# Kernel optimization log

Hardware: AMD Instinct MI355X
Metric: run time of the kernel (lower is better)

## Reference

```python
import jax, jax.numpy as jnp
import numpy as np

B, T, IN_DIM = 32, 1024, 32
E, H, P = 256, 4, 32  # embed_dim, heads, max_patches
HD = E // H


def _lin(x, w, b):
    # torch nn.Linear: y = x @ W.T + b, W: [out, in]
    return jnp.einsum('...i,oi->...o', x, w) + b


def setup_inputs() -> dict:
    key = jax.random.key(0)
    ks = jax.random.split(key, 13)
    s = 0.02
    return {
        'x': jax.random.normal(ks[0], (B, T, IN_DIM), jnp.float32),
        'ip_w': jax.random.normal(ks[1], (E, IN_DIM), jnp.float32) * s,
        'ip_b': jnp.zeros((E,), jnp.float32),
        'in_proj_w': jax.random.normal(ks[2], (3 * E, E), jnp.float32) * s,
        'in_proj_b': jnp.zeros((3 * E,), jnp.float32),
        'out_w': jax.random.normal(ks[3], (E, E), jnp.float32) * s,
        'out_b': jnp.zeros((E,), jnp.float32),
        'bp_w1': jax.random.normal(ks[4], (32, E), jnp.float32) * s,
        'bp_b1': jnp.zeros((32,), jnp.float32),
        'bp_w2': jax.random.normal(ks[5], (1, 32), jnp.float32) * s,
        'bp_b2': jnp.zeros((1,), jnp.float32),
        'pr_w': jax.random.normal(ks[6], (E, E), jnp.float32) * s,
        'pr_b': jnp.zeros((E,), jnp.float32),
    }


def reference(x, ip_w, ip_b, in_proj_w, in_proj_b, out_w, out_b,
              bp_w1, bp_b1, bp_w2, bp_b2, pr_w, pr_b):
    # input projection
    h = _lin(x, ip_w, ip_b)  # [B,T,E]
    # MultiheadAttention (self-attn, batch_first, eval/no-dropout)
    qkv = _lin(h, in_proj_w, in_proj_b)  # [B,T,3E]
    q, k, v = jnp.split(qkv, 3, axis=-1)
    q = q.reshape(B, T, H, HD)
    k = k.reshape(B, T, H, HD)
    v = v.reshape(B, T, H, HD)
    scores = jnp.einsum('bqhd,bkhd->bhqk', q, k) / jnp.sqrt(jnp.float32(HD))
    attn = jax.nn.softmax(scores, axis=-1)
    ctx = jnp.einsum('bhqk,bkhd->bqhd', attn, v).reshape(B, T, E)
    attn_out = _lin(ctx, out_w, out_b)  # [B,T,E]
    # boundary scores
    bscore = jax.nn.sigmoid(_lin(jax.nn.relu(_lin(attn_out, bp_w1, bp_b1)), bp_w2, bp_b2))[..., 0]  # [B,T]
    cbp = jnp.cumsum(bscore, axis=1)
    cbp = cbp / (cbp[:, -1:] + 1e-6)
    pid = jnp.minimum(jnp.floor(cbp * P).astype(jnp.int32), P - 1)  # [B,T]
    # segment-mean pooling via scatter-add
    b_idx = jnp.broadcast_to(jnp.arange(B)[:, None], (B, T))
    pe = jnp.zeros((B, P, E), attn_out.dtype).at[b_idx, pid].add(attn_out)
    cnt = jnp.zeros((B, P), attn_out.dtype).at[b_idx, pid].add(1.0)
    pe = pe / jnp.clip(cnt, 1.0)[..., None]
    return _lin(pe, pr_w, pr_b)  # [B,P,E]
```

## Files before the change

kernel.cpp:

```cpp
#include <hip/hip_runtime.h>
#include <math.h>

constexpr int Bn  = 32;
constexpr int Tn  = 1024;
constexpr int INn = 32;
constexpr int En  = 256;
constexpr int Pn  = 32;

typedef short bf16x8 __attribute__((ext_vector_type(8)));
typedef float f32x4  __attribute__((ext_vector_type(4)));

__device__ __forceinline__ unsigned short f2bf(float f) {
    unsigned int b = __float_as_uint(f);
    b += 0x7FFF + ((b >> 16) & 1);
    return (unsigned short)(b >> 16);
}
__device__ __forceinline__ float bf2f(unsigned short h) {
    return __uint_as_float(((unsigned int)h) << 16);
}
__device__ __forceinline__ unsigned int permpack(float lo, float hi) {
    return __builtin_amdgcn_perm(__float_as_uint(hi), __float_as_uint(lo),
                                 0x07060302u);
}

__global__ __launch_bounds__(256) void k_prep(const float* __restrict__ ipw,
                                              const float* __restrict__ ipb,
                                              const float* __restrict__ inw,
                                              const float* __restrict__ inb,
                                              const float* __restrict__ outw,
                                              const float* __restrict__ w1,
                                              const float* __restrict__ prw,
                                              unsigned short* __restrict__ Wcb,
                                              float* __restrict__ bc,
                                              unsigned short* __restrict__ Wb,
                                              unsigned short* __restrict__ w1h,
                                              unsigned short* __restrict__ w1l,
                                              unsigned short* __restrict__ pwh,
                                              unsigned short* __restrict__ pwl) {
    int blk = blockIdx.x, tid = threadIdx.x;
    if (blk < 96) {
        int idx = blk * 256 + tid;
        int o = idx >> 5, i = idx & 31;
        const float* wr = inw + (size_t)o * En;
        float a0 = 0.f, a1 = 0.f;
        for (int e = 0; e < En; e += 2) {
            a0 += wr[e]     * ipw[(size_t)e * INn + i];
            a1 += wr[e + 1] * ipw[(size_t)(e + 1) * INn + i];
        }
        Wcb[(size_t)o * INn + i] = f2bf(a0 + a1);
    } else if (blk < 99) {
        int o = (blk - 96) * 256 + tid;
        const float* wr = inw + (size_t)o * En;
        float a = inb[o];
        for (int e = 0; e < En; ++e) a += wr[e] * ipb[e];
        bc[o] = a;
    } else if (blk < 163) {
        int idx = (blk - 99) * 256 + tid;
        float4 a = *(const float4*)(outw + (size_t)idx * 4);
        unsigned int u0 = f2bf(a.x) | ((unsigned int)f2bf(a.y) << 16);
        unsigned int u1 = f2bf(a.z) | ((unsigned int)f2bf(a.w) << 16);
        *(uint2*)(Wb + (size_t)idx * 4) = make_uint2(u0, u1);
    } else if (blk < 195) {
        int idx = (blk - 163) * 256 + tid;
        float a = w1[idx];
        unsigned short h = f2bf(a);
        w1h[idx] = h;
        w1l[idx] = f2bf(a - bf2f(h));
    } else {
        int idx = (blk - 195) * 256 + tid;
        float a = prw[idx];
        unsigned short h = f2bf(a);
        pwh[idx] = h;
        pwl[idx] = f2bf(a - bf2f(h));
    }
}

__global__ __launch_bounds__(256, 2) void k_qkv(const float* __restrict__ x,
                                                const unsigned short* __restrict__ Wcb,
                                                const float* __restrict__ bc,
                                                unsigned short* __restrict__ Qb,
                                                unsigned short* __restrict__ Kb,
                                                unsigned short* __restrict__ Vt) {
    int tid = threadIdx.x;
    int wv = tid >> 6, lane = tid & 63;
    int cl = lane & 15, quad = lane >> 4;
    int m0 = blockIdx.x * 64;
    int b = m0 >> 10, tl0 = m0 & 1023;
    int n0w = wv * 192;
    f32x4 zero4 = {0.f, 0.f, 0.f, 0.f};

    bf16x8 wfrag[12]; float bv[12];
#pragma unroll
    for (int nt = 0; nt < 12; ++nt) {
        int col = n0w + nt * 16 + cl;
        wfrag[nt] = *(const bf16x8*)(Wcb + (size_t)col * 32 + quad * 8);
        bv[nt] = bc[col];
    }
#pragma unroll
    for (int mt = 0; mt < 4; ++mt) {
        const float* xr = x + (size_t)(m0 + mt * 16 + cl) * 32 + quad * 8;
        float4 xa = *(const float4*)xr, xc = *(const float4*)(xr + 4);
        bf16x8 af;
        af[0] = (short)f2bf(xa.x); af[1] = (short)f2bf(xa.y);
        af[2] = (short)f2bf(xa.z); af[3] = (short)f2bf(xa.w);
        af[4] = (short)f2bf(xc.x); af[5] = (short)f2bf(xc.y);
        af[6] = (short)f2bf(xc.z); af[7] = (short)f2bf(xc.w);
        f32x4 acc[12];
#pragma unroll
        for (int nt = 0; nt < 12; ++nt)
            acc[nt] = __builtin_amdgcn_mfma_f32_16x16x32_bf16(af, wfrag[nt], zero4, 0, 0, 0);
        int tloc = tl0 + mt * 16 + quad * 4;
#pragma unroll
        for (int nt = 0; nt < 12; ++nt) {
            int col = n0w + nt * 16 + cl;
            int slot = col >> 8, c = col & 255;
            int h = c >> 6, d = c & 63;
            int bh = b * 4 + h;
            if (slot == 2) {
                unsigned int u0 = f2bf(acc[nt][0] + bv[nt]) |
                                  ((unsigned int)f2bf(acc[nt][1] + bv[nt]) << 16);
                unsigned int u1 = f2bf(acc[nt][2] + bv[nt]) |
                                  ((unsigned int)f2bf(acc[nt][3] + bv[nt]) << 16);
                *(uint2*)(Vt + ((size_t)bh * 64 + d) * 1024 + tloc) = make_uint2(u0, u1);
            } else {
                unsigned short* dst = (slot ? Kb : Qb) +
                                      ((size_t)bh * 1024 + tloc) * 64 + d;
#pragma unroll
                for (int r = 0; r < 4; ++r)
                    dst[(size_t)r * 64] = f2bf(acc[nt][r] + bv[nt]);
            }
        }
    }
}

__global__ __launch_bounds__(256, 4) void k_attn(const unsigned short* __restrict__ Qb,
                                                 const unsigned short* __restrict__ Kb,
                                                 const unsigned short* __restrict__ Vt,
                                                 unsigned short* __restrict__ Po0,
                                                 unsigned short* __restrict__ Po1,
                                                 float* __restrict__ L0,
                                                 float* __restrict__ L1) {
    __shared__ unsigned short Ks[64][72];
    __shared__ unsigned short Vs[64][72];
    __shared__ __align__(16) unsigned short Pl[4][2][16][40];
    int blk = blockIdx.x;
    int bh = blk & 127;
    int r_ = blk >> 7;
    int qb = r_ & 7, half = r_ >> 3;
    int b = bh >> 2, h = bh & 3;
    int tid = threadIdx.x;
    int wv = tid >> 6, lane = tid & 63;
    int cl = lane & 15, quad = lane >> 4;
    int qbase = qb * 128 + wv * 32;

    f32x4 zero4 = {0.f, 0.f, 0.f, 0.f};
    bf16x8 qfrag[2][2];
#pragma unroll
    for (int tt = 0; tt < 2; ++tt)
#pragma unroll
        for (int ch = 0; ch < 2; ++ch)
            qfrag[tt][ch] = *(const bf16x8*)(Qb +
                ((size_t)bh * 1024 + qbase + tt * 16 + cl) * 64 + ch * 32 + quad * 8);
    f32x4 acc[2][4];
#pragma unroll
    for (int tt = 0; tt < 2; ++tt)
#pragma unroll
        for (int dt = 0; dt < 4; ++dt) acc[tt][dt] = zero4;
    float l[2] = {0.f, 0.f};

    const unsigned short* Kbase = Kb + (size_t)bh * 65536;
    const unsigned short* Vbase = Vt + (size_t)bh * 65536;

    for (int kt = 0; kt < 8; ++kt) {
        int ktt = half * 8 + kt;
#pragma unroll
        for (int r = 0; r < 2; ++r) {
            int idx = r * 256 + tid; int row = idx >> 3, c16 = idx & 7;
            *(uint4*)&Ks[row][c16 * 8] =
                *(const uint4*)(Kbase + (size_t)(ktt * 64 + row) * 64 + c16 * 8);
            *(uint4*)&Vs[row][c16 * 8] =
                *(const uint4*)(Vbase + (size_t)row * 1024 + ktt * 64 + c16 * 8);
        }
        __syncthreads();
#pragma unroll
        for (int c = 0; c < 2; ++c) {
            bf16x8 ka0 = *(const bf16x8*)&Ks[c * 32 + cl][quad * 8];
            bf16x8 ka1 = *(const bf16x8*)&Ks[c * 32 + cl][32 + quad * 8];
            bf16x8 kb0 = *(const bf16x8*)&Ks[c * 32 + 16 + cl][quad * 8];
            bf16x8 kb1 = *(const bf16x8*)&Ks[c * 32 + 16 + cl][32 + quad * 8];
            bf16x8 va[4];
#pragma unroll
            for (int dt = 0; dt < 4; ++dt)
                va[dt] = *(const bf16x8*)&Vs[dt * 16 + cl][c * 32 + quad * 8];
#pragma unroll
            for (int tt = 0; tt < 2; ++tt) {
                f32x4 s0 = __builtin_amdgcn_mfma_f32_16x16x32_bf16(ka0, qfrag[tt][0], zero4, 0, 0, 0);
                s0 = __builtin_amdgcn_mfma_f32_16x16x32_bf16(ka1, qfrag[tt][1], s0, 0, 0, 0);
                f32x4 s1 = __builtin_amdgcn_mfma_f32_16x16x32_bf16(kb0, qfrag[tt][0], zero4, 0, 0, 0);
                s1 = __builtin_amdgcn_mfma_f32_16x16x32_bf16(kb1, qfrag[tt][1], s1, 0, 0, 0);
                float p0 = __expf(0.125f * s0[0]), p1 = __expf(0.125f * s0[1]);
                float p2 = __expf(0.125f * s0[2]), p3 = __expf(0.125f * s0[3]);
                float p4 = __expf(0.125f * s1[0]), p5 = __expf(0.125f * s1[1]);
                float p6 = __expf(0.125f * s1[2]), p7 = __expf(0.125f * s1[3]);
                unsigned int w0 = permpack(p0, p1);
                unsigned int w1 = permpack(p2, p3);
                unsigned int w2 = permpack(p4, p5);
                unsigned int w3 = permpack(p6, p7);
                l[tt] += ((__uint_as_float(w0 << 16) + __uint_as_float(w0 & 0xffff0000u)) +
                          (__uint_as_float(w1 << 16) + __uint_as_float(w1 & 0xffff0000u))) +
                         ((__uint_as_float(w2 << 16) + __uint_as_float(w2 & 0xffff0000u)) +
                          (__uint_as_float(w3 << 16) + __uint_as_float(w3 & 0xffff0000u)));
                *(uint2*)&Pl[wv][tt][cl][quad * 4]      = make_uint2(w0, w1);
                *(uint2*)&Pl[wv][tt][cl][16 + quad * 4] = make_uint2(w2, w3);
            }
            asm volatile("s_waitcnt lgkmcnt(0)" ::: "memory");
#pragma unroll
            for (int tt = 0; tt < 2; ++tt) {
                bf16x8 pf = *(const bf16x8*)&Pl[wv][tt][cl][quad * 8];
#pragma unroll
                for (int dt = 0; dt < 4; ++dt)
                    acc[tt][dt] = __builtin_amdgcn_mfma_f32_16x16x32_bf16(pf, va[dt], acc[tt][dt], 0, 0, 0);
            }
        }
        __syncthreads();
    }
#pragma unroll
    for (int tt = 0; tt < 2; ++tt) {
        l[tt] += __shfl_xor(l[tt], 16);
        l[tt] += __shfl_xor(l[tt], 32);
    }
    unsigned short* Po = half ? Po1 : Po0;
    float* Lp = half ? L1 : L0;
#pragma unroll
    for (int tt = 0; tt < 2; ++tt) {
#pragma unroll
        for (int r = 0; r < 4; ++r) {
            size_t row = (size_t)(b * 1024 + qbase + tt * 16 + quad * 4 + r) * En;
#pragma unroll
            for (int dt = 0; dt < 4; ++dt)
                Po[row + h * 64 + dt * 16 + cl] = f2bf(acc[tt][dt][r]);
        }
    }
    if (quad == 0) {
#pragma unroll
        for (int tt = 0; tt < 2; ++tt)
            Lp[bh * 1024 + qbase + tt * 16 + cl] = l[tt];
    }
}

__global__ __launch_bounds__(256) void k_out(const unsigned short* __restrict__ Po0,
                                             const unsigned short* __restrict__ Po1,
                                             const float* __restrict__ L0,
                                             const float* __restrict__ L1,
                                             const unsigned short* __restrict__ Wb,
                                             const float* __restrict__ bias,
                                             float* __restrict__ AO) {
    __shared__ unsigned short As[64][32];
    __shared__ unsigned short Bs[256][32];
    int tid = threadIdx.x;
    int wv = tid >> 6, lane = tid & 63;
    int cl = lane & 15, quad = lane >> 4;
    size_t m0 = (size_t)blockIdx.x * 64;

    f32x4 acc[4][4];
#pragma unroll
    for (int mt = 0; mt < 4; ++mt)
#pragma unroll
        for (int nt = 0; nt < 4; ++nt) acc[mt][nt] = {0.f, 0.f, 0.f, 0.f};

    for (int kt = 0; kt < 8; ++kt) {
        if (kt) __syncthreads();
        {
            int row = tid >> 2, c4 = tid & 3;
            size_t g = (m0 + row) * En + kt * 32 + c4 * 8;
            uint4 u0 = *(const uint4*)(Po0 + g);
            uint4 u1 = *(const uint4*)(Po1 + g);
            int gt = (int)(m0 + row);
            int li = ((gt >> 10) * 4 + (kt >> 1)) * 1024 + (gt & 1023);
            float linv = 1.f / (L0[li] + L1[li]);
            unsigned int a0[4] = {u0.x, u0.y, u0.z, u0.w};
            unsigned int a1[4] = {u1.x, u1.y, u1.z, u1.w};
            unsigned int w[4];
#pragma unroll
            for (int j = 0; j < 4; ++j) {
                float lo = (bf2f((unsigned short)(a0[j] & 0xffff)) +
                            bf2f((unsigned short)(a1[j] & 0xffff))) * linv;
                float hi = (bf2f((unsigned short)(a0[j] >> 16)) +
                            bf2f((unsigned short)(a1[j] >> 16))) * linv;
                w[j] = f2bf(lo) | ((unsigned int)f2bf(hi) << 16);
            }
            *(uint4*)&As[row][c4 * 8] = make_uint4(w[0], w[1], w[2], w[3]);
        }
#pragma unroll
        for (int j = 0; j < 4; ++j) {
            int lin = j * 256 + tid; int n = lin >> 2, c = lin & 3;
            *(uint4*)&Bs[n][c * 8] =
                *(const uint4*)(Wb + (size_t)n * En + kt * 32 + c * 8);
        }
        __syncthreads();
        bf16x8 af[4], bfr[4];
#pragma unroll
        for (int mt = 0; mt < 4; ++mt)
            af[mt] = *(const bf16x8*)&As[mt * 16 + cl][quad * 8];
#pragma unroll
        for (int nt = 0; nt < 4; ++nt)
            bfr[nt] = *(const bf16x8*)&Bs[wv * 64 + nt * 16 + cl][quad * 8];
#pragma unroll
        for (int mt = 0; mt < 4; ++mt)
#pragma unroll
            for (int nt = 0; nt < 4; ++nt)
                acc[mt][nt] = __builtin_amdgcn_mfma_f32_16x16x32_bf16(af[mt], bfr[nt], acc[mt][nt], 0, 0, 0);
    }
    float bv[4];
#pragma unroll
    for (int nt = 0; nt < 4; ++nt) bv[nt] = bias[wv * 64 + nt * 16 + cl];
#pragma unroll
    for (int mt = 0; mt < 4; ++mt)
#pragma unroll
        for (int nt = 0; nt < 4; ++nt)
#pragma unroll
            for (int r = 0; r < 4; ++r)
                AO[(m0 + mt * 16 + quad * 4 + r) * En + wv * 64 + nt * 16 + cl] =
                    acc[mt][nt][r] + bv[nt];
}

__global__ __launch_bounds__(256) void k_bscore(const float* __restrict__ AO,
                                                const unsigned short* __restrict__ w1h,
                                                const unsigned short* __restrict__ w1l,
                                                const float* __restrict__ b1,
                                                const float* __restrict__ w2,
                                                const float* __restrict__ b2,
                                                float* __restrict__ bsc) {
    __shared__ unsigned short Ah[128][72];
    __shared__ unsigned short Al[128][72];
    int tid = threadIdx.x;
    int wv = tid >> 6, lane = tid & 63;
    int cl = lane & 15, quad = lane >> 4;
    int m0 = blockIdx.x * 128;

    f32x4 acc[2][2];
#pragma unroll
    for (int mt = 0; mt < 2; ++mt)
#pragma unroll
        for (int nt = 0; nt < 2; ++nt) acc[mt][nt] = {0.f, 0.f, 0.f, 0.f};

    for (int kt = 0; kt < 4; ++kt) {
        if (kt) __syncthreads();
#pragma unroll
        for (int j = 0; j < 8; ++j) {
            int lin = j * 256 + tid; int row = lin >> 4, c4 = lin & 15;
            float4 a = *(const float4*)(AO + (size_t)(m0 + row) * En + kt * 64 + c4 * 4);
            unsigned short h0 = f2bf(a.x), h1v = f2bf(a.y), h2 = f2bf(a.z), h3 = f2bf(a.w);
            unsigned short l0 = f2bf(a.x - bf2f(h0)), l1v = f2bf(a.y - bf2f(h1v));
            unsigned short l2 = f2bf(a.z - bf2f(h2)), l3 = f2bf(a.w - bf2f(h3));
            *(uint2*)&Ah[row][c4 * 4] =
                make_uint2(h0 | ((unsigned int)h1v << 16), h2 | ((unsigned int)h3 << 16));
            *(uint2*)&Al[row][c4 * 4] =
                make_uint2(l0 | ((unsigned int)l1v << 16), l2 | ((unsigned int)l3 << 16));
        }
        __syncthreads();
#pragma unroll
        for (int ks = 0; ks < 2; ++ks) {
            bf16x8 bh_[2], bl_[2];
#pragma unroll
            for (int nt = 0; nt < 2; ++nt) {
                size_t off = (size_t)(nt * 16 + cl) * En + kt * 64 + ks * 32 + quad * 8;
                bh_[nt] = *(const bf16x8*)(w1h + off);
                bl_[nt] = *(const bf16x8*)(w1l + off);
            }
#pragma unroll
            for (int mt = 0; mt < 2; ++mt) {
                int row = wv * 32 + mt * 16 + cl;
                bf16x8 ah = *(const bf16x8*)&Ah[row][ks * 32 + quad * 8];
                bf16x8 al = *(const bf16x8*)&Al[row][ks * 32 + quad * 8];
#pragma unroll
                for (int nt = 0; nt < 2; ++nt) {
                    acc[mt][nt] = __builtin_amdgcn_mfma_f32_16x16x32_bf16(ah, bh_[nt], acc[mt][nt], 0, 0, 0);
                    acc[mt][nt] = __builtin_amdgcn_mfma_f32_16x16x32_bf16(ah, bl_[nt], acc[mt][nt], 0, 0, 0);
                    acc[mt][nt] = __builtin_amdgcn_mfma_f32_16x16x32_bf16(al, bh_[nt], acc[mt][nt], 0, 0, 0);
                }
            }
        }
    }
    float b1v[2], w2v[2];
#pragma unroll
    for (int nt = 0; nt < 2; ++nt) {
        b1v[nt] = b1[nt * 16 + cl];
        w2v[nt] = w2[nt * 16 + cl];
    }
    float b2v = b2[0];
#pragma unroll
    for (int mt = 0; mt < 2; ++mt) {
        f32x4 z;
#pragma unroll
        for (int r = 0; r < 4; ++r)
            z[r] = fmaxf(acc[mt][0][r] + b1v[0], 0.f) * w2v[0] +
                   fmaxf(acc[mt][1][r] + b1v[1], 0.f) * w2v[1];
#pragma unroll
        for (int d = 1; d < 16; d <<= 1)
#pragma unroll
            for (int r = 0; r < 4; ++r) z[r] += __shfl_xor(z[r], d);
        if (cl == 0) {
#pragma unroll
            for (int r = 0; r < 4; ++r)
                bsc[m0 + wv * 32 + mt * 16 + quad * 4 + r] =
                    1.f / (1.f + __expf(-(z[r] + b2v)));
        }
    }
}

__global__ __launch_bounds__(1024) void k_scan(const float* __restrict__ bsc,
                                               int* __restrict__ segs) {
    __shared__ float wsum[16];
    __shared__ float s_pre[1024];
    __shared__ float s_tot;
    int b = blockIdx.x, t = threadIdx.x;
    float x = bsc[b * Tn + t];
#pragma unroll
    for (int d = 1; d < 64; d <<= 1) {
        float y = __shfl_up(x, d);
        if ((t & 63) >= d) x += y;
    }
    int w = t >> 6;
    if ((t & 63) == 63) wsum[w] = x;
    __syncthreads();
    if (t == 0) {
        float s = 0.f;
        for (int i = 0; i < 16; ++i) { float tmp = wsum[i]; wsum[i] = s; s += tmp; }
        s_tot = s;
    }
    __syncthreads();
    float pre = x + wsum[w];
    s_pre[t] = pre;
    __syncthreads();
    float denom = s_tot + 1e-6f;
    float qv = pre / denom * 32.0f;
    int pid = min((int)floorf(qv), 31);
    int pidprev = -1;
    if (t > 0) {
        float qp = s_pre[t - 1] / denom * 32.0f;
        pidprev = min((int)floorf(qp), 31);
    }
    for (int p = pidprev + 1; p <= pid; ++p) segs[b * 33 + p] = t;
    if (t == 1023)
        for (int p = pid + 1; p <= 32; ++p) segs[b * 33 + p] = Tn;
}

__global__ __launch_bounds__(256) void k_pool(const float* __restrict__ ao,
                                              const int* __restrict__ segs,
                                              float* __restrict__ PE) {
    int b = blockIdx.y, p = blockIdx.x;
    int s = segs[b * 33 + p];
    int e = segs[b * 33 + p + 1];
    int tid = threadIdx.x;
    float sum = 0.f;
    for (int t = s; t < e; ++t)
        sum += ao[((size_t)b * Tn + t) * En + tid];
    PE[(size_t)(b * Pn + p) * En + tid] = sum / fmaxf((float)(e - s), 1.f);
}

__global__ __launch_bounds__(256) void k_final(const float* __restrict__ PE,
                                               const unsigned short* __restrict__ pwh,
                                               const unsigned short* __restrict__ pwl,
                                               const float* __restrict__ prb,
                                               float* __restrict__ out) {
    __shared__ unsigned short Ah[64][40];
    __shared__ unsigned short Al[64][40];
    int tid = threadIdx.x;
    int wv = tid >> 6, lane = tid & 63;
    int cl = lane & 15, quad = lane >> 4;
    int m0 = blockIdx.x * 64;

    f32x4 acc[4][4];
#pragma unroll
    for (int mt = 0; mt < 4; ++mt)
#pragma unroll
        for (int nt = 0; nt < 4; ++nt) acc[mt][nt] = {0.f, 0.f, 0.f, 0.f};

    for (int kt = 0; kt < 8; ++kt) {
        if (kt) __syncthreads();
        {
            int row = tid >> 2, c8 = (tid & 3) * 8;
            const float* src = PE + (size_t)(m0 + row) * En + kt * 32 + c8;
            float4 a = *(const float4*)src, b4 = *(const float4*)(src + 4);
            float v[8] = {a.x, a.y, a.z, a.w, b4.x, b4.y, b4.z, b4.w};
            unsigned int hw[4], lw[4];
#pragma unroll
            for (int j = 0; j < 4; ++j) {
                unsigned short h0 = f2bf(v[2 * j]), h1 = f2bf(v[2 * j + 1]);
                unsigned short q0 = f2bf(v[2 * j] - bf2f(h0));
                unsigned short q1 = f2bf(v[2 * j + 1] - bf2f(h1));
                hw[j] = h0 | ((unsigned int)h1 << 16);
                lw[j] = q0 | ((unsigned int)q1 << 16);
            }
            *(uint4*)&Ah[row][c8] = make_uint4(hw[0], hw[1], hw[2], hw[3]);
            *(uint4*)&Al[row][c8] = make_uint4(lw[0], lw[1], lw[2], lw[3]);
        }
        __syncthreads();
        bf16x8 ah[4], al[4], bh_[4], bl_[4];
#pragma unroll
        for (int mt = 0; mt < 4; ++mt) {
            ah[mt] = *(const bf16x8*)&Ah[mt * 16 + cl][quad * 8];
            al[mt] = *(const bf16x8*)&Al[mt * 16 + cl][quad * 8];
        }
#pragma unroll
        for (int nt = 0; nt < 4; ++nt) {
            size_t off = (size_t)(wv * 64 + nt * 16 + cl) * En + kt * 32 + quad * 8;
            bh_[nt] = *(const bf16x8*)(pwh + off);
            bl_[nt] = *(const bf16x8*)(pwl + off);
        }
#pragma unroll
        for (int mt = 0; mt < 4; ++mt)
#pragma unroll
            for (int nt = 0; nt < 4; ++nt) {
                acc[mt][nt] = __builtin_amdgcn_mfma_f32_16x16x32_bf16(ah[mt], bh_[nt], acc[mt][nt], 0, 0, 0);
                acc[mt][nt] = __builtin_amdgcn_mfma_f32_16x16x32_bf16(ah[mt], bl_[nt], acc[mt][nt], 0, 0, 0);
                acc[mt][nt] = __builtin_amdgcn_mfma_f32_16x16x32_bf16(al[mt], bh_[nt], acc[mt][nt], 0, 0, 0);
            }
    }
    float bv[4];
#pragma unroll
    for (int nt = 0; nt < 4; ++nt) bv[nt] = prb[wv * 64 + nt * 16 + cl];
#pragma unroll
    for (int mt = 0; mt < 4; ++mt)
#pragma unroll
        for (int nt = 0; nt < 4; ++nt)
#pragma unroll
            for (int r = 0; r < 4; ++r)
                out[(size_t)(m0 + mt * 16 + quad * 4 + r) * En + wv * 64 + nt * 16 + cl] =
                    acc[mt][nt][r] + bv[nt];
}

extern "C" void kernel_launch(void* const* d_in, const int* in_sizes, int n_in,
                              void* d_out, int out_size, void* d_ws, size_t ws_size,
                              hipStream_t stream) {
    const float* x    = (const float*)d_in[0];
    const float* ipw  = (const float*)d_in[1];
    const float* ipb  = (const float*)d_in[2];
    const float* inw  = (const float*)d_in[3];
    const float* inb  = (const float*)d_in[4];
    const float* outw = (const float*)d_in[5];
    const float* outb = (const float*)d_in[6];
    const float* bw1  = (const float*)d_in[7];
    const float* bb1  = (const float*)d_in[8];
    const float* bw2  = (const float*)d_in[9];
    const float* bb2  = (const float*)d_in[10];
    const float* prw  = (const float*)d_in[11];
    const float* prb  = (const float*)d_in[12];

    char* base = (char*)d_ws;
    unsigned short* Qb  = (unsigned short*)base;
    unsigned short* Kb  = Qb + (size_t)8388608;
    float*          AO  = (float*)base;
    unsigned short* Vt  = (unsigned short*)(base + (size_t)33554432);
    float*          PE  = (float*)(base + (size_t)33554432);
    unsigned short* Po0 = (unsigned short*)(base + (size_t)50331648);
    unsigned short* Po1 = (unsigned short*)(base + (size_t)67108864);
    unsigned short* Wcb = (unsigned short*)(base + (size_t)83886080);
    float*          bc  = (float*)(base + (size_t)83935232);
    unsigned short* Wb  = (unsigned short*)(base + (size_t)83938304);
    unsigned short* w1h = (unsigned short*)(base + (size_t)84069376);
    unsigned short* w1l = (unsigned short*)(base + (size_t)84085760);
    float*          L0  = (float*)(base + (size_t)84102144);
    float*          L1  = (float*)(base + (size_t)84626432);
    float*          bsc = (float*)(base + (size_t)85150720);
    int*           segs = (int*)(base + (size_t)85281792);
    unsigned short* pwh = (unsigned short*)(base + (size_t)85286912);
    unsigned short* pwl = (unsigned short*)(base + (size_t)85417984);

    k_prep<<<451, 256, 0, stream>>>(ipw, ipb, inw, inb, outw, bw1, prw,
                                    Wcb, bc, Wb, w1h, w1l, pwh, pwl);
    k_qkv<<<512, 256, 0, stream>>>(x, Wcb, bc, Qb, Kb, Vt);
    k_attn<<<2048, 256, 0, stream>>>(Qb, Kb, Vt, Po0, Po1, L0, L1);
    k_out<<<512, 256, 0, stream>>>(Po0, Po1, L0, L1, Wb, outb, AO);
    k_bscore<<<256, 256, 0, stream>>>(AO, w1h, w1l, bb1, bw2, bb2, bsc);
    k_scan<<<32, 1024, 0, stream>>>(bsc, segs);
    k_pool<<<dim3(32, 32), 256, 0, stream>>>(AO, segs, PE);
    k_final<<<16, 256, 0, stream>>>(PE, pwh, pwl, prb, (float*)d_out);
}
```

Before: 218.0 us.

## Fuse boundary MLP into out-proj, scan into pool, weight casts into qkv

```diff
diff --git a/kernel.cpp b/kernel.cpp
--- a/kernel.cpp
+++ b/kernel.cpp
@@ -27,16 +27,8 @@
                                               const float* __restrict__ ipb,
                                               const float* __restrict__ inw,
                                               const float* __restrict__ inb,
-                                              const float* __restrict__ outw,
-                                              const float* __restrict__ w1,
-                                              const float* __restrict__ prw,
                                               unsigned short* __restrict__ Wcb,
-                                              float* __restrict__ bc,
-                                              unsigned short* __restrict__ Wb,
-                                              unsigned short* __restrict__ w1h,
-                                              unsigned short* __restrict__ w1l,
-                                              unsigned short* __restrict__ pwh,
-                                              unsigned short* __restrict__ pwl) {
+                                              float* __restrict__ bc) {
     int blk = blockIdx.x, tid = threadIdx.x;
     if (blk < 96) {
         int idx = blk * 256 + tid;
@@ -48,40 +40,53 @@
             a1 += wr[e + 1] * ipw[(size_t)(e + 1) * INn + i];
         }
         Wcb[(size_t)o * INn + i] = f2bf(a0 + a1);
-    } else if (blk < 99) {
+    } else {
         int o = (blk - 96) * 256 + tid;
         const float* wr = inw + (size_t)o * En;
         float a = inb[o];
         for (int e = 0; e < En; ++e) a += wr[e] * ipb[e];
         bc[o] = a;
-    } else if (blk < 163) {
-        int idx = (blk - 99) * 256 + tid;
-        float4 a = *(const float4*)(outw + (size_t)idx * 4);
-        unsigned int u0 = f2bf(a.x) | ((unsigned int)f2bf(a.y) << 16);
-        unsigned int u1 = f2bf(a.z) | ((unsigned int)f2bf(a.w) << 16);
-        *(uint2*)(Wb + (size_t)idx * 4) = make_uint2(u0, u1);
-    } else if (blk < 195) {
-        int idx = (blk - 163) * 256 + tid;
-        float a = w1[idx];
-        unsigned short h = f2bf(a);
-        w1h[idx] = h;
-        w1l[idx] = f2bf(a - bf2f(h));
-    } else {
-        int idx = (blk - 195) * 256 + tid;
-        float a = prw[idx];
-        unsigned short h = f2bf(a);
-        pwh[idx] = h;
-        pwl[idx] = f2bf(a - bf2f(h));
     }
 }
 
 __global__ __launch_bounds__(256, 2) void k_qkv(const float* __restrict__ x,
                                                 const unsigned short* __restrict__ Wcb,
                                                 const float* __restrict__ bc,
+                                                const float* __restrict__ outw,
+                                                const float* __restrict__ w1,
+                                                const float* __restrict__ prw,
                                                 unsigned short* __restrict__ Qb,
                                                 unsigned short* __restrict__ Kb,
-                                                unsigned short* __restrict__ Vt) {
+                                                unsigned short* __restrict__ Vt,
+                                                unsigned short* __restrict__ Wb,
+                                                unsigned short* __restrict__ w1h,
+                                                unsigned short* __restrict__ w1l,
+                                                unsigned short* __restrict__ pwh,
+                                                unsigned short* __restrict__ pwl) {
     int tid = threadIdx.x;
+    if (blockIdx.x >= 512) {
+        int cb = blockIdx.x - 512;
+        if (cb < 64) {
+            int idx = cb * 256 + tid;
+            float4 a = *(const float4*)(outw + (size_t)idx * 4);
+            unsigned int u0 = f2bf(a.x) | ((unsigned int)f2bf(a.y) << 16);
+            unsigned int u1 = f2bf(a.z) | ((unsigned int)f2bf(a.w) << 16);
+            *(uint2*)(Wb + (size_t)idx * 4) = make_uint2(u0, u1);
+        } else if (cb < 96) {
+            int idx = (cb - 64) * 256 + tid;
+            float a = w1[idx];
+            unsigned short h = f2bf(a);
+            w1h[idx] = h;
+            w1l[idx] = f2bf(a - bf2f(h));
+        } else {
+            int idx = (cb - 96) * 256 + tid;
+            float a = prw[idx];
+            unsigned short h = f2bf(a);
+            pwh[idx] = h;
+            pwl[idx] = f2bf(a - bf2f(h));
+        }
+        return;
+    }
     int wv = tid >> 6, lane = tid & 63;
     int cl = lane & 15, quad = lane >> 4;
     int m0 = blockIdx.x * 64;
@@ -152,6 +157,7 @@
     int wv = tid >> 6, lane = tid & 63;
     int cl = lane & 15, quad = lane >> 4;
     int qbase = qb * 128 + wv * 32;
+    const float SCL = 0.18033688f;
 
     f32x4 zero4 = {0.f, 0.f, 0.f, 0.f};
     bf16x8 qfrag[2][2];
@@ -198,10 +204,10 @@
                 s0 = __builtin_amdgcn_mfma_f32_16x16x32_bf16(ka1, qfrag[tt][1], s0, 0, 0, 0);
                 f32x4 s1 = __builtin_amdgcn_mfma_f32_16x16x32_bf16(kb0, qfrag[tt][0], zero4, 0, 0, 0);
                 s1 = __builtin_amdgcn_mfma_f32_16x16x32_bf16(kb1, qfrag[tt][1], s1, 0, 0, 0);
-                float p0 = __expf(0.125f * s0[0]), p1 = __expf(0.125f * s0[1]);
-                float p2 = __expf(0.125f * s0[2]), p3 = __expf(0.125f * s0[3]);
-                float p4 = __expf(0.125f * s1[0]), p5 = __expf(0.125f * s1[1]);
-                float p6 = __expf(0.125f * s1[2]), p7 = __expf(0.125f * s1[3]);
+                float p0 = exp2f(SCL * s0[0]), p1 = exp2f(SCL * s0[1]);
+                float p2 = exp2f(SCL * s0[2]), p3 = exp2f(SCL * s0[3]);
+                float p4 = exp2f(SCL * s1[0]), p5 = exp2f(SCL * s1[1]);
+                float p6 = exp2f(SCL * s1[2]), p7 = exp2f(SCL * s1[3]);
                 unsigned int w0 = permpack(p0, p1);
                 unsigned int w1 = permpack(p2, p3);
                 unsigned int w2 = permpack(p4, p5);
@@ -254,9 +260,16 @@
                                              const float* __restrict__ L1,
                                              const unsigned short* __restrict__ Wb,
                                              const float* __restrict__ bias,
-                                             float* __restrict__ AO) {
+                                             const unsigned short* __restrict__ w1h,
+                                             const unsigned short* __restrict__ w1l,
+                                             const float* __restrict__ b1,
+                                             const float* __restrict__ w2,
+                                             const float* __restrict__ b2,
+                                             float* __restrict__ AO,
+                                             float* __restrict__ bsc) {
     __shared__ unsigned short As[64][32];
     __shared__ unsigned short Bs[256][32];
+    __shared__ unsigned short Ah[64][258];
     int tid = threadIdx.x;
     int wv = tid >> 6, lane = tid & 63;
     int cl = lane & 15, quad = lane >> 4;
@@ -314,88 +327,39 @@
     float bv[4];
 #pragma unroll
     for (int nt = 0; nt < 4; ++nt) bv[nt] = bias[wv * 64 + nt * 16 + cl];
+    __syncthreads();
 #pragma unroll
     for (int mt = 0; mt < 4; ++mt)
 #pragma unroll
         for (int nt = 0; nt < 4; ++nt)
 #pragma unroll
-            for (int r = 0; r < 4; ++r)
-                AO[(m0 + mt * 16 + quad * 4 + r) * En + wv * 64 + nt * 16 + cl] =
-                    acc[mt][nt][r] + bv[nt];
-}
-
-__global__ __launch_bounds__(256) void k_bscore(const float* __restrict__ AO,
-                                                const unsigned short* __restrict__ w1h,
-                                                const unsigned short* __restrict__ w1l,
-                                                const float* __restrict__ b1,
-                                                const float* __restrict__ w2,
-                                                const float* __restrict__ b2,
-                                                float* __restrict__ bsc) {
-    __shared__ unsigned short Ah[128][72];
-    __shared__ unsigned short Al[128][72];
-    int tid = threadIdx.x;
-    int wv = tid >> 6, lane = tid & 63;
-    int cl = lane & 15, quad = lane >> 4;
-    int m0 = blockIdx.x * 128;
-
-    f32x4 acc[2][2];
-#pragma unroll
-    for (int mt = 0; mt < 2; ++mt)
-#pragma unroll
-        for (int nt = 0; nt < 2; ++nt) acc[mt][nt] = {0.f, 0.f, 0.f, 0.f};
-
-    for (int kt = 0; kt < 4; ++kt) {
-        if (kt) __syncthreads();
-#pragma unroll
-        for (int j = 0; j < 8; ++j) {
-            int lin = j * 256 + tid; int row = lin >> 4, c4 = lin & 15;
-            float4 a = *(const float4*)(AO + (size_t)(m0 + row) * En + kt * 64 + c4 * 4);
-            unsigned short h0 = f2bf(a.x), h1v = f2bf(a.y), h2 = f2bf(a.z), h3 = f2bf(a.w);
-            unsigned short l0 = f2bf(a.x - bf2f(h0)), l1v = f2bf(a.y - bf2f(h1v));
-            unsigned short l2 = f2bf(a.z - bf2f(h2)), l3 = f2bf(a.w - bf2f(h3));
-            *(uint2*)&Ah[row][c4 * 4] =
-                make_uint2(h0 | ((unsigned int)h1v << 16), h2 | ((unsigned int)h3 << 16));
-            *(uint2*)&Al[row][c4 * 4] =
-                make_uint2(l0 | ((unsigned int)l1v << 16), l2 | ((unsigned int)l3 << 16));
-        }
-        __syncthreads();
-#pragma unroll
-        for (int ks = 0; ks < 2; ++ks) {
-            bf16x8 bh_[2], bl_[2];
+            for (int r = 0; r < 4; ++r) {
+                float a = acc[mt][nt][r] + bv[nt];
+                AO[(m0 + mt * 16 + quad * 4 + r) * En + wv * 64 + nt * 16 + cl] = a;
+                Ah[mt * 16 + quad * 4 + r][wv * 64 + nt * 16 + cl] = f2bf(a);
+            }
+    __syncthreads();
+    {
+        f32x4 hacc[2] = {{0.f, 0.f, 0.f, 0.f}, {0.f, 0.f, 0.f, 0.f}};
+        for (int kt = 0; kt < 8; ++kt) {
+            bf16x8 ah = *(const bf16x8*)&Ah[wv * 16 + cl][kt * 32 + quad * 8];
 #pragma unroll
             for (int nt = 0; nt < 2; ++nt) {
-                size_t off = (size_t)(nt * 16 + cl) * En + kt * 64 + ks * 32 + quad * 8;
-                bh_[nt] = *(const bf16x8*)(w1h + off);
-                bl_[nt] = *(const bf16x8*)(w1l + off);
-            }
-#pragma unroll
-            for (int mt = 0; mt < 2; ++mt) {
-                int row = wv * 32 + mt * 16 + cl;
-                bf16x8 ah = *(const bf16x8*)&Ah[row][ks * 32 + quad * 8];
-                bf16x8 al = *(const bf16x8*)&Al[row][ks * 32 + quad * 8];
-#pragma unroll
-                for (int nt = 0; nt < 2; ++nt) {
-                    acc[mt][nt] = __builtin_amdgcn_mfma_f32_16x16x32_bf16(ah, bh_[nt], acc[mt][nt], 0, 0, 0);
-                    acc[mt][nt] = __builtin_amdgcn_mfma_f32_16x16x32_bf16(ah, bl_[nt], acc[mt][nt], 0, 0, 0);
-                    acc[mt][nt] = __builtin_amdgcn_mfma_f32_16x16x32_bf16(al, bh_[nt], acc[mt][nt], 0, 0, 0);
-                }
-            }
-        }
-    }
-    float b1v[2], w2v[2];
-#pragma unroll
-    for (int nt = 0; nt < 2; ++nt) {
-        b1v[nt] = b1[nt * 16 + cl];
-        w2v[nt] = w2[nt * 16 + cl];
-    }
-    float b2v = b2[0];
-#pragma unroll
-    for (int mt = 0; mt < 2; ++mt) {
+                size_t off = (size_t)(nt * 16 + cl) * En + kt * 32 + quad * 8;
+                bf16x8 bh_ = *(const bf16x8*)(w1h + off);
+                bf16x8 bl_ = *(const bf16x8*)(w1l + off);
+                hacc[nt] = __builtin_amdgcn_mfma_f32_16x16x32_bf16(ah, bh_, hacc[nt], 0, 0, 0);
+                hacc[nt] = __builtin_amdgcn_mfma_f32_16x16x32_bf16(ah, bl_, hacc[nt], 0, 0, 0);
+            }
+        }
+        float b1v[2] = {b1[cl], b1[16 + cl]};
+        float w2v[2] = {w2[cl], w2[16 + cl]};
+        float b2v = b2[0];
         f32x4 z;
 #pragma unroll
         for (int r = 0; r < 4; ++r)
-            z[r] = fmaxf(acc[mt][0][r] + b1v[0], 0.f) * w2v[0] +
-                   fmaxf(acc[mt][1][r] + b1v[1], 0.f) * w2v[1];
+            z[r] = fmaxf(hacc[0][r] + b1v[0], 0.f) * w2v[0] +
+                   fmaxf(hacc[1][r] + b1v[1], 0.f) * w2v[1];
 #pragma unroll
         for (int d = 1; d < 16; d <<= 1)
 #pragma unroll
@@ -403,60 +367,62 @@
         if (cl == 0) {
 #pragma unroll
             for (int r = 0; r < 4; ++r)
-                bsc[m0 + wv * 32 + mt * 16 + quad * 4 + r] =
+                bsc[m0 + wv * 16 + quad * 4 + r] =
                     1.f / (1.f + __expf(-(z[r] + b2v)));
         }
     }
 }
 
-__global__ __launch_bounds__(1024) void k_scan(const float* __restrict__ bsc,
-                                               int* __restrict__ segs) {
-    __shared__ float wsum[16];
-    __shared__ float s_pre[1024];
-    __shared__ float s_tot;
-    int b = blockIdx.x, t = threadIdx.x;
-    float x = bsc[b * Tn + t];
+__global__ __launch_bounds__(256) void k_pool(const float* __restrict__ bsc,
+                                              const float* __restrict__ AO,
+                                              float* __restrict__ PE) {
+    __shared__ float pre[1024];
+    __shared__ float wsl[4];
+    __shared__ float stot_s;
+    __shared__ int   segs[33];
+    int b = blockIdx.y, p = blockIdx.x, t = threadIdx.x;
+    int lane = t & 63, wv = t >> 6;
+    float4 v = *(const float4*)(bsc + b * 1024 + t * 4);
+    float s0 = v.x, s1 = s0 + v.y, s2 = s1 + v.z, s3 = s2 + v.w;
+    float ts = s3, sc = ts;
 #pragma unroll
     for (int d = 1; d < 64; d <<= 1) {
-        float y = __shfl_up(x, d);
-        if ((t & 63) >= d) x += y;
-    }
-    int w = t >> 6;
-    if ((t & 63) == 63) wsum[w] = x;
+        float y = __shfl_up(sc, d);
+        if (lane >= d) sc += y;
+    }
+    if (lane == 63) wsl[wv] = sc;
     __syncthreads();
     if (t == 0) {
         float s = 0.f;
-        for (int i = 0; i < 16; ++i) { float tmp = wsum[i]; wsum[i] = s; s += tmp; }
-        s_tot = s;
+        for (int i = 0; i < 4; ++i) { float tmp = wsl[i]; wsl[i] = s; s += tmp; }
+        stot_s = s;
     }
     __syncthreads();
-    float pre = x + wsum[w];
-    s_pre[t] = pre;
+    float base = wsl[wv] + (sc - ts);
+    pre[t * 4 + 0] = base + s0;
+    pre[t * 4 + 1] = base + s1;
+    pre[t * 4 + 2] = base + s2;
+    pre[t * 4 + 3] = base + s3;
     __syncthreads();
-    float denom = s_tot + 1e-6f;
-    float qv = pre / denom * 32.0f;
-    int pid = min((int)floorf(qv), 31);
-    int pidprev = -1;
-    if (t > 0) {
-        float qp = s_pre[t - 1] / denom * 32.0f;
-        pidprev = min((int)floorf(qp), 31);
-    }
-    for (int p = pidprev + 1; p <= pid; ++p) segs[b * 33 + p] = t;
-    if (t == 1023)
-        for (int p = pid + 1; p <= 32; ++p) segs[b * 33 + p] = Tn;
-}
-
-__global__ __launch_bounds__(256) void k_pool(const float* __restrict__ ao,
-                                              const int* __restrict__ segs,
-                                              float* __restrict__ PE) {
-    int b = blockIdx.y, p = blockIdx.x;
-    int s = segs[b * 33 + p];
-    int e = segs[b * 33 + p + 1];
-    int tid = threadIdx.x;
+    float denom = stot_s + 1e-6f;
+    int lastpid = 0;
+#pragma unroll
+    for (int i = 0; i < 4; ++i) {
+        int t4 = t * 4 + i;
+        int pid = min((int)floorf(pre[t4] / denom * 32.0f), 31);
+        int pidprev = (t4 == 0) ? -1
+                      : min((int)floorf(pre[t4 - 1] / denom * 32.0f), 31);
+        for (int pp = pidprev + 1; pp <= pid; ++pp) segs[pp] = t4;
+        lastpid = pid;
+    }
+    if (t == 255)
+        for (int pp = lastpid + 1; pp <= 32; ++pp) segs[pp] = Tn;
+    __syncthreads();
+    int s = segs[p], e = segs[p + 1];
     float sum = 0.f;
-    for (int t = s; t < e; ++t)
-        sum += ao[((size_t)b * Tn + t) * En + tid];
-    PE[(size_t)(b * Pn + p) * En + tid] = sum / fmaxf((float)(e - s), 1.f);
+    for (int tk = s; tk < e; ++tk)
+        sum += AO[((size_t)b * Tn + tk) * En + t];
+    PE[(size_t)(b * Pn + p) * En + t] = sum / fmaxf((float)(e - s), 1.f);
 }
 
 __global__ __launch_bounds__(256) void k_final(const float* __restrict__ PE,
@@ -464,8 +430,8 @@
                                                const unsigned short* __restrict__ pwl,
                                                const float* __restrict__ prb,
                                                float* __restrict__ out) {
-    __shared__ unsigned short Ah[64][40];
-    __shared__ unsigned short Al[64][40];
+    __shared__ unsigned short Ahs[64][40];
+    __shared__ unsigned short Als[64][40];
     int tid = threadIdx.x;
     int wv = tid >> 6, lane = tid & 63;
     int cl = lane & 15, quad = lane >> 4;
@@ -493,15 +459,15 @@
                 hw[j] = h0 | ((unsigned int)h1 << 16);
                 lw[j] = q0 | ((unsigned int)q1 << 16);
             }
-            *(uint4*)&Ah[row][c8] = make_uint4(hw[0], hw[1], hw[2], hw[3]);
-            *(uint4*)&Al[row][c8] = make_uint4(lw[0], lw[1], lw[2], lw[3]);
+            *(uint4*)&Ahs[row][c8] = make_uint4(hw[0], hw[1], hw[2], hw[3]);
+            *(uint4*)&Als[row][c8] = make_uint4(lw[0], lw[1], lw[2], lw[3]);
         }
         __syncthreads();
         bf16x8 ah[4], al[4], bh_[4], bl_[4];
 #pragma unroll
         for (int mt = 0; mt < 4; ++mt) {
-            ah[mt] = *(const bf16x8*)&Ah[mt * 16 + cl][quad * 8];
-            al[mt] = *(const bf16x8*)&Al[mt * 16 + cl][quad * 8];
+            ah[mt] = *(const bf16x8*)&Ahs[mt * 16 + cl][quad * 8];
+            al[mt] = *(const bf16x8*)&Als[mt * 16 + cl][quad * 8];
         }
 #pragma unroll
         for (int nt = 0; nt < 4; ++nt) {
@@ -564,17 +530,15 @@
     float*          L0  = (float*)(base + (size_t)84102144);
     float*          L1  = (float*)(base + (size_t)84626432);
     float*          bsc = (float*)(base + (size_t)85150720);
-    int*           segs = (int*)(base + (size_t)85281792);
     unsigned short* pwh = (unsigned short*)(base + (size_t)85286912);
     unsigned short* pwl = (unsigned short*)(base + (size_t)85417984);
 
-    k_prep<<<451, 256, 0, stream>>>(ipw, ipb, inw, inb, outw, bw1, prw,
-                                    Wcb, bc, Wb, w1h, w1l, pwh, pwl);
-    k_qkv<<<512, 256, 0, stream>>>(x, Wcb, bc, Qb, Kb, Vt);
+    k_prep<<<99, 256, 0, stream>>>(ipw, ipb, inw, inb, Wcb, bc);
+    k_qkv<<<864, 256, 0, stream>>>(x, Wcb, bc, outw, bw1, prw,
+                                   Qb, Kb, Vt, Wb, w1h, w1l, pwh, pwl);
     k_attn<<<2048, 256, 0, stream>>>(Qb, Kb, Vt, Po0, Po1, L0, L1);
-    k_out<<<512, 256, 0, stream>>>(Po0, Po1, L0, L1, Wb, outb, AO);
-    k_bscore<<<256, 256, 0, stream>>>(AO, w1h, w1l, bb1, bw2, bb2, bsc);
-    k_scan<<<32, 1024, 0, stream>>>(bsc, segs);
-    k_pool<<<dim3(32, 32), 256, 0, stream>>>(AO, segs, PE);
+    k_out<<<512, 256, 0, stream>>>(Po0, Po1, L0, L1, Wb, outb,
+                                   w1h, w1l, bb1, bw2, bb2, AO, bsc);
+    k_pool<<<dim3(32, 32), 256, 0, stream>>>(bsc, AO, PE);
     k_final<<<16, 256, 0, stream>>>(PE, pwh, pwl, prb, (float*)d_out);
 }
```

New measurement: 217.0 us. Within noise of the previous version (-0.5%).
